# Optimization experiments

Hardware: AMD Instinct MI355X
Metric: run time of the kernel (lower is better)

## Reference

```python
import jax, jax.numpy as jnp
import numpy as np

B, T, N = 128, 20, 49
VOCAB, EMB, HDIM, VDIM, ATT = 10000, 512, 1024, 512, 512
LN_EPS = 1e-5


def _layer_norm(x, g, b):
    mu = x.mean(-1, keepdims=True)
    var = ((x - mu) ** 2).mean(-1, keepdims=True)
    return (x - mu) * jax.lax.rsqrt(var + LN_EPS) * g + b


def _lstm_cell(x, h, c, Wih, Whh, bih, bhh):
    gates = x @ Wih.T + h @ Whh.T + bih + bhh  # [B, 4H]
    i, f, g, o = jnp.split(gates, 4, axis=-1)  # torch LSTMCell gate order
    c_new = jax.nn.sigmoid(f) * c + jax.nn.sigmoid(i) * jnp.tanh(g)
    h_new = jax.nn.sigmoid(o) * jnp.tanh(c_new)
    return h_new, c_new


def setup_inputs() -> dict:
    key = jax.random.key(0)
    ks = jax.random.split(key, 16)
    w = lambda k, shape: (jax.random.normal(k, shape, jnp.float32) * 0.02)
    embed_W = w(ks[2], (VOCAB, EMB)).at[0].set(0.0)  # padding_idx=0 row is zeros
    return dict(
        V=jax.random.normal(ks[0], (B, N, VDIM), jnp.float32),
        y=jax.random.randint(ks[1], (B, T), 0, VOCAB),
        embed_W=embed_W,
        Vp_W=w(ks[3], (HDIM, VDIM)), Vp_b=jnp.zeros((HDIM,), jnp.float32),
        attW=w(ks[4], (ATT, HDIM)), attU=w(ks[5], (ATT, HDIM)), attv=w(ks[6], (1, ATT)),
        l1_Wih=w(ks[7], (4 * HDIM, EMB + HDIM)), l1_Whh=w(ks[8], (4 * HDIM, HDIM)),
        l1_bih=jnp.zeros((4 * HDIM,), jnp.float32), l1_bhh=jnp.zeros((4 * HDIM,), jnp.float32),
        l2_Wih=w(ks[9], (4 * HDIM, HDIM)), l2_Whh=w(ks[10], (4 * HDIM, HDIM)),
        l2_bih=jnp.zeros((4 * HDIM,), jnp.float32), l2_bhh=jnp.zeros((4 * HDIM,), jnp.float32),
        n1_g=jnp.ones((HDIM,), jnp.float32), n1_b=jnp.zeros((HDIM,), jnp.float32),
        n2_g=jnp.ones((HDIM,), jnp.float32), n2_b=jnp.zeros((HDIM,), jnp.float32),
        ih_W=w(ks[11], (HDIM, HDIM)), ih_b=jnp.zeros((HDIM,), jnp.float32),
        ic_W=w(ks[12], (HDIM, HDIM)), ic_b=jnp.zeros((HDIM,), jnp.float32),
        proj_W=w(ks[13], (EMB, HDIM)),
    )


def reference(V, y, embed_W, Vp_W, Vp_b, attW, attU, attv,
              l1_Wih, l1_Whh, l1_bih, l1_bhh,
              l2_Wih, l2_Whh, l2_bih, l2_bhh,
              n1_g, n1_b, n2_g, n2_b,
              ih_W, ih_b, ic_W, ic_b, proj_W):
    Vp = V @ Vp_W.T + Vp_b                      # [B, N, H]
    feat_mean = Vp.mean(1)                      # [B, H]
    h1 = jnp.tanh(feat_mean @ ih_W.T + ih_b)
    c1 = jnp.tanh(feat_mean @ ic_W.T + ic_b)
    h2 = jnp.zeros_like(h1)
    c2 = jnp.zeros_like(c1)

    Uv = Vp @ attU.T                            # [B, N, ATT] (hoisted out of loop)
    emb_y = embed_W[y]                          # [B, T, EMB]
    xs = jnp.swapaxes(emb_y[:, :-1], 0, 1)      # [T-1, B, EMB]

    def step(carry, x_t):
        h1, c1, h2, c2 = carry
        # additive attention (dropout is identity in eval)
        e = jnp.tanh((h2 @ attW.T)[:, None, :] + Uv) @ attv[0]   # [B, N]
        a = jax.nn.softmax(e, axis=1)
        ctx = jnp.einsum('bn,bnh->bh', a, Vp)
        h1n, c1n = _lstm_cell(jnp.concatenate([x_t, ctx], -1), h1, c1,
                              l1_Wih, l1_Whh, l1_bih, l1_bhh)
        h1n = _layer_norm(h1n, n1_g, n1_b)
        h2n, c2n = _lstm_cell(h1n, h2, c2, l2_Wih, l2_Whh, l2_bih, l2_bhh)
        h2n = _layer_norm(h2n, n2_g, n2_b)
        logit = (h2n @ proj_W.T) @ embed_W.T    # [B, VOCAB]
        return (h1n, c1n, h2n, c2n), logit

    _, logits = jax.lax.scan(step, (h1, c1, h2, c2), xs)
    return jnp.swapaxes(logits, 0, 1)           # [B, T-1, VOCAB]
```

## Files before the change

### kernel.cpp

```cpp
#include <hip/hip_runtime.h>
#include <hip/hip_bf16.h>

#define TSTEPS 19

typedef short bf16x8 __attribute__((ext_vector_type(8)));
typedef short bf16x4 __attribute__((ext_vector_type(4)));
typedef float f32x4 __attribute__((ext_vector_type(4)));

__device__ __forceinline__ f32x4 mfma_bf16(bf16x8 a, bf16x8 b, f32x4 c) {
    return __builtin_amdgcn_mfma_f32_16x16x32_bf16(a, b, c, 0, 0, 0);
}
__device__ __forceinline__ short f2b(float f) {
    union { float f; unsigned u; } v; v.f = f;
    unsigned r = v.u + 0x7fffu + ((v.u >> 16) & 1u);
    return (short)(r >> 16);
}
__device__ __forceinline__ float b2f(short s) {
    union { unsigned u; float f; } v; v.u = ((unsigned)(unsigned short)s) << 16;
    return v.f;
}
__device__ __forceinline__ float sigm(float x) { return 1.f / (1.f + __expf(-x)); }
__device__ __forceinline__ float tanhfast(float x) { return 1.f - 2.f / (__expf(2.f * x) + 1.f); }

__global__ __launch_bounds__(256) void k_convert(
    const float* __restrict__ l1_Wih, const float* __restrict__ l1_Whh,
    const float* __restrict__ l2_Wih, const float* __restrict__ l2_Whh,
    const float* __restrict__ embed_W, const float* __restrict__ proj_W,
    const float* __restrict__ attW, const float* __restrict__ ih_W,
    const float* __restrict__ ic_W, const float* __restrict__ Vp_W,
    const float* __restrict__ attU, const float* __restrict__ V,
    const int* __restrict__ y, const float* __restrict__ n1g,
    const float* __restrict__ n2g,
    short* __restrict__ l1h, short* __restrict__ l1l,
    short* __restrict__ l2h, short* __restrict__ l2l,
    short* __restrict__ embB, short* __restrict__ pa, short* __restrict__ ihic,
    short* __restrict__ VpWh, short* __restrict__ VpWl, short* __restrict__ attUb,
    short* __restrict__ Vbh, short* __restrict__ Vbl, short* __restrict__ xall) {
    const int N1 = 4096 * 2560, N2 = 4096 * 2048, N3 = 10000 * 512, N4 = 1024 * 1024,
              N5 = 2048 * 1024, N6 = 1024 * 512, N7 = 512 * 1024, N8 = 128 * 49 * 512,
              N9 = 19 * 128 * 512;
    const int total4 = (N1 + N2 + N3 + N4 + N5 + N6 + N7 + N8 + N9) >> 2;
    int stride = gridDim.x * blockDim.x;
    for (int g = blockIdx.x * blockDim.x + threadIdx.x; g < total4; g += stride) {
        int e = g << 2;
        if (e < N1) {
            int n = e / 2560, k = e - n * 2560;
            f32x4 v;
            if (k < 1536) {
                v = *(const f32x4*)(l1_Wih + (size_t)n * 1536 + k);
            } else {
                f32x4 w = *(const f32x4*)(l1_Whh + (size_t)n * 1024 + (k - 1536));
                f32x4 gg = *(const f32x4*)(n1g + (k - 1536));
#pragma unroll
                for (int j = 0; j < 4; j++) v[j] = gg[j] * w[j];
            }
            bf16x4 hi, lo;
#pragma unroll
            for (int j = 0; j < 4; j++) { hi[j] = f2b(v[j]); lo[j] = f2b(v[j] - b2f(hi[j])); }
            *(bf16x4*)(l1h + e) = hi; *(bf16x4*)(l1l + e) = lo; continue;
        }
        e -= N1;
        if (e < N2) {
            int n = e >> 11, k = e & 2047;
            f32x4 w, gg;
            if (k < 1024) {
                w = *(const f32x4*)(l2_Wih + (size_t)n * 1024 + k);
                gg = *(const f32x4*)(n1g + k);
            } else {
                w = *(const f32x4*)(l2_Whh + (size_t)n * 1024 + (k - 1024));
                gg = *(const f32x4*)(n2g + (k - 1024));
            }
            bf16x4 hi, lo;
#pragma unroll
            for (int j = 0; j < 4; j++) {
                float v = gg[j] * w[j];
                hi[j] = f2b(v); lo[j] = f2b(v - b2f(hi[j]));
            }
            *(bf16x4*)(l2h + e) = hi; *(bf16x4*)(l2l + e) = lo; continue;
        }
        e -= N2;
        if (e < N3) {
            f32x4 v = *(const f32x4*)(embed_W + e);
            bf16x4 o;
#pragma unroll
            for (int j = 0; j < 4; j++) o[j] = f2b(v[j]);
            *(bf16x4*)(embB + e) = o; continue;
        }
        e -= N3;
        if (e < N4) {
            int n = e >> 10, k = e & 1023;
            f32x4 w = (n < 512) ? *(const f32x4*)(proj_W + (size_t)n * 1024 + k)
                                : *(const f32x4*)(attW + (size_t)(n - 512) * 1024 + k);
            f32x4 gg = *(const f32x4*)(n2g + k);
            bf16x4 o;
#pragma unroll
            for (int j = 0; j < 4; j++) o[j] = f2b(gg[j] * w[j]);
            *(bf16x4*)(pa + e) = o; continue;
        }
        e -= N4;
        if (e < N5) {
            int n = e >> 10, k = e & 1023;
            f32x4 w = (n < 1024) ? *(const f32x4*)(ih_W + (size_t)n * 1024 + k)
                                 : *(const f32x4*)(ic_W + (size_t)(n - 1024) * 1024 + k);
            bf16x4 o;
#pragma unroll
            for (int j = 0; j < 4; j++) o[j] = f2b(w[j]);
            *(bf16x4*)(ihic + e) = o; continue;
        }
        e -= N5;
        if (e < N6) {
            f32x4 v = *(const f32x4*)(Vp_W + e);
            bf16x4 hi, lo;
#pragma unroll
            for (int j = 0; j < 4; j++) { hi[j] = f2b(v[j]); lo[j] = f2b(v[j] - b2f(hi[j])); }
            *(bf16x4*)(VpWh + e) = hi; *(bf16x4*)(VpWl + e) = lo; continue;
        }
        e -= N6;
        if (e < N7) {
            f32x4 v = *(const f32x4*)(attU + e);
            bf16x4 o;
#pragma unroll
            for (int j = 0; j < 4; j++) o[j] = f2b(v[j]);
            *(bf16x4*)(attUb + e) = o; continue;
        }
        e -= N7;
        if (e < N8) {
            f32x4 v = *(const f32x4*)(V + e);
            bf16x4 hi, lo;
#pragma unroll
            for (int j = 0; j < 4; j++) { hi[j] = f2b(v[j]); lo[j] = f2b(v[j] - b2f(hi[j])); }
            *(bf16x4*)(Vbh + e) = hi; *(bf16x4*)(Vbl + e) = lo; continue;
        }
        e -= N8;
        {
            int t = e >> 16; int r = e & 65535;
            int b = r >> 9, k = r & 511;
            int idx = y[b * 20 + t];
            f32x4 v = *(const f32x4*)(embed_W + (size_t)idx * 512 + k);
            bf16x4 o;
#pragma unroll
            for (int j = 0; j < 4; j++) o[j] = f2b(v[j]);
            *(bf16x4*)(xall + e) = o;
        }
    }
}

__global__ __launch_bounds__(256) void k_corr(
    const float* __restrict__ l1_Whh, const float* __restrict__ l2_Wih,
    const float* __restrict__ l2_Whh, const float* __restrict__ proj_W,
    const float* __restrict__ attW,
    const float* __restrict__ n1g, const float* __restrict__ n1b,
    const float* __restrict__ n2g, const float* __restrict__ n2b,
    float* __restrict__ wg1, float* __restrict__ wb1,
    float* __restrict__ wg2a, float* __restrict__ wb2a,
    float* __restrict__ wg2b, float* __restrict__ wb2b,
    float* __restrict__ wgp, float* __restrict__ wbp) {
    int w = (blockIdx.x * 256 + threadIdx.x) >> 6;
    int lane = threadIdx.x & 63;
    if (w >= 13312) return;
    const float* row; const float* g; const float* b; float* og; float* ob;
    if (w < 4096)       { row = l1_Whh + (size_t)w * 1024; g = n1g; b = n1b; og = wg1 + w; ob = wb1 + w; }
    else if (w < 8192)  { int j = w - 4096; row = l2_Wih + (size_t)j * 1024; g = n1g; b = n1b; og = wg2a + j; ob = wb2a + j; }
    else if (w < 12288) { int j = w - 8192; row = l2_Whh + (size_t)j * 1024; g = n2g; b = n2b; og = wg2b + j; ob = wb2b + j; }
    else                { int j = w - 12288;
                          row = (j < 512) ? proj_W + (size_t)j * 1024 : attW + (size_t)(j - 512) * 1024;
                          g = n2g; b = n2b; og = wgp + j; ob = wbp + j; }
    float sg = 0.f, sb = 0.f;
    for (int k = lane; k < 1024; k += 64) { float wv = row[k]; sg += g[k] * wv; sb += b[k] * wv; }
#pragma unroll
    for (int o = 1; o < 64; o <<= 1) { sg += __shfl_xor(sg, o); sb += __shfl_xor(sb, o); }
    if (lane == 0) { *og = sg; *ob = sb; }
}

__device__ __forceinline__ void gemm_core(const short* __restrict__ A, int lda,
                                          const short* __restrict__ Bm, int ldb,
                                          int mb, int n0, int K, int Nlim,
                                          f32x4 acc[2][4]) {
    int lane = threadIdx.x & 63, wave = threadIdx.x >> 6;
    int col = lane & 15, quad = lane >> 4;
    const short* a0p = A + (size_t)(mb + wave * 32 + col) * lda + quad * 8;
    const short* a1p = a0p + (size_t)16 * lda;
    const short* bp[4];
#pragma unroll
    for (int s = 0; s < 4; s++) {
        int n = n0 + s * 16 + col;
        if (n >= Nlim) n = 0;
        bp[s] = Bm + (size_t)n * ldb + quad * 8;
    }
    for (int kb = 0; kb < K; kb += 32) {
        bf16x8 a0 = *(const bf16x8*)(a0p + kb);
        bf16x8 a1 = *(const bf16x8*)(a1p + kb);
#pragma unroll
        for (int s = 0; s < 4; s++) {
            bf16x8 b = *(const bf16x8*)(bp[s] + kb);
            acc[0][s] = mfma_bf16(a0, b, acc[0][s]);
            acc[1][s] = mfma_bf16(a1, b, acc[1][s]);
        }
    }
}

__global__ __launch_bounds__(256) void k_gemm_vp(const short* __restrict__ Ah,
                                                 const short* __restrict__ Al,
                                                 const short* __restrict__ Bh,
                                                 const short* __restrict__ Bl,
                                                 const float* __restrict__ Vp_b,
                                                 short* __restrict__ Vph,
                                                 short* __restrict__ Vpl) {
    __shared__ alignas(16) short Bs[2 * 64 * 256];
    char* Bsb = (char*)Bs;
    int tid = threadIdx.x, lane = tid & 63, wave = tid >> 6, col = lane & 15, quad = lane >> 4;
    int mb = blockIdx.y * 128, n0 = blockIdx.x * 64;
    f32x4 acc[2][4] = {};
    const short* ah0 = Ah + (size_t)(mb + wave * 32 + col) * 512 + quad * 8;
    const short* al0 = Al + (size_t)(mb + wave * 32 + col) * 512 + quad * 8;
    const short* ah1 = ah0 + 16 * 512; const short* al1 = al0 + 16 * 512;
#pragma unroll
    for (int ph = 0; ph < 2; ph++) {
        int kbase = ph * 256;
        __syncthreads();
#pragma unroll
        for (int i = 0; i < 8; i++) {
            int r = i * 8 + wave * 2 + (lane >> 5);
            int n = n0 + r;
            int e = (lane & 31) * 8;
            bf16x8 vh = *(const bf16x8*)(Bh + (size_t)n * 512 + kbase + e);
            bf16x8 vl = *(const bf16x8*)(Bl + (size_t)n * 512 + kbase + e);
            int wo = r * 512 + ((e * 2) ^ ((r & 7) << 4));
            *(bf16x8*)(Bsb + wo) = vh;
            *(bf16x8*)(Bsb + 32768 + wo) = vl;
        }
        __syncthreads();
        for (int kb = 0; kb < 256; kb += 32) {
            bf16x8 h0 = *(const bf16x8*)(ah0 + kbase + kb), l0 = *(const bf16x8*)(al0 + kbase + kb);
            bf16x8 h1 = *(const bf16x8*)(ah1 + kbase + kb), l1 = *(const bf16x8*)(al1 + kbase + kb);
#pragma unroll
            for (int s = 0; s < 4; s++) {
                int r = s * 16 + col;
                int off = r * 512 + ((quad * 16 + kb * 2) ^ ((r & 7) << 4));
                bf16x8 wh = *(const bf16x8*)(Bsb + off);
                bf16x8 wl = *(const bf16x8*)(Bsb + 32768 + off);
                acc[0][s] = mfma_bf16(h0, wh, acc[0][s]);
                acc[0][s] = mfma_bf16(l0, wh, acc[0][s]);
                acc[0][s] = mfma_bf16(h0, wl, acc[0][s]);
                acc[1][s] = mfma_bf16(h1, wh, acc[1][s]);
                acc[1][s] = mfma_bf16(l1, wh, acc[1][s]);
                acc[1][s] = mfma_bf16(h1, wl, acc[1][s]);
            }
        }
    }
#pragma unroll
    for (int i = 0; i < 2; i++)
#pragma unroll
        for (int s = 0; s < 4; s++) {
            int n = n0 + s * 16 + col;
            float bias = Vp_b[n];
#pragma unroll
            for (int r = 0; r < 4; r++) {
                int m = mb + wave * 32 + i * 16 + quad * 4 + r;
                float v = acc[i][s][r] + bias;
                short hi = f2b(v);
                Vph[(size_t)m * 1024 + n] = hi;
                Vpl[(size_t)m * 1024 + n] = f2b(v - b2f(hi));
            }
        }
}

__global__ __launch_bounds__(256) void k_gemm_uv(const short* __restrict__ Vph,
                                                 const short* __restrict__ Vpl,
                                                 const short* __restrict__ attUb,
                                                 short* __restrict__ Uv) {
    __shared__ alignas(16) short Bs[64 * 512];
    char* Bsb = (char*)Bs;
    int tid = threadIdx.x, lane = tid & 63, wave = tid >> 6, col = lane & 15, quad = lane >> 4;
    int mb = blockIdx.y * 128, n0 = blockIdx.x * 64;
    f32x4 acc[2][4] = {};
    const short* ah0 = Vph + (size_t)(mb + wave * 32 + col) * 1024 + quad * 8;
    const short* al0 = Vpl + (size_t)(mb + wave * 32 + col) * 1024 + quad * 8;
    const short* ah1 = ah0 + 16 * 1024; const short* al1 = al0 + 16 * 1024;
#pragma unroll
    for (int ph = 0; ph < 2; ph++) {
        int kbase = ph * 512;
        __syncthreads();
#pragma unroll
        for (int i = 0; i < 16; i++) {
            int r = i * 4 + wave;
            int n = n0 + r;
            int e = lane * 8;
            bf16x8 v = *(const bf16x8*)(attUb + (size_t)n * 1024 + kbase + e);
            *(bf16x8*)(Bsb + r * 1024 + ((e * 2) ^ ((r & 7) << 4))) = v;
        }
        __syncthreads();
        for (int kb = 0; kb < 512; kb += 32) {
            bf16x8 h0 = *(const bf16x8*)(ah0 + kbase + kb), l0 = *(const bf16x8*)(al0 + kbase + kb);
            bf16x8 h1 = *(const bf16x8*)(ah1 + kbase + kb), l1 = *(const bf16x8*)(al1 + kbase + kb);
#pragma unroll
            for (int s = 0; s < 4; s++) {
                int r = s * 16 + col;
                bf16x8 b = *(const bf16x8*)(Bsb + r * 1024 + ((quad * 16 + kb * 2) ^ ((r & 7) << 4)));
                acc[0][s] = mfma_bf16(h0, b, acc[0][s]);
                acc[0][s] = mfma_bf16(l0, b, acc[0][s]);
                acc[1][s] = mfma_bf16(h1, b, acc[1][s]);
                acc[1][s] = mfma_bf16(l1, b, acc[1][s]);
            }
        }
    }
#pragma unroll
    for (int i = 0; i < 2; i++)
#pragma unroll
        for (int s = 0; s < 4; s++) {
            int n = n0 + s * 16 + col;
#pragma unroll
            for (int r = 0; r < 4; r++) {
                int m = mb + wave * 32 + i * 16 + quad * 4 + r;
                Uv[(size_t)m * 512 + n] = f2b(acc[i][s][r]);
            }
        }
}

__global__ __launch_bounds__(256) void k_gemm_xpart(const short* __restrict__ xall,
                                                    const short* __restrict__ l1h,
                                                    float* __restrict__ xpart) {
    f32x4 acc[2][4] = {};
    int mb = blockIdx.y * 128, n0 = blockIdx.x * 64;
    gemm_core(xall, 512, l1h, 2560, mb, n0, 512, 1 << 30, acc);
    int lane = threadIdx.x & 63, wave = threadIdx.x >> 6, col = lane & 15, quad = lane >> 4;
#pragma unroll
    for (int i = 0; i < 2; i++)
#pragma unroll
        for (int s = 0; s < 4; s++) {
            int n = n0 + s * 16 + col;
#pragma unroll
            for (int r = 0; r < 4; r++) {
                int m = mb + wave * 32 + i * 16 + quad * 4 + r;
                xpart[(size_t)m * 4096 + n] = acc[i][s][r];
            }
        }
}

__global__ __launch_bounds__(256) void k_feat(const short* __restrict__ Vph,
                                              const short* __restrict__ Vpl,
                                              short* __restrict__ feat,
                                              float* __restrict__ c2,
                                              short* __restrict__ h2h1,
                                              short* __restrict__ h2l1,
                                              float* __restrict__ st1,
                                              float* __restrict__ st2) {
    int b = blockIdx.x, tid = threadIdx.x;
    int h0 = tid * 4;
    float acc[4] = {0.f, 0.f, 0.f, 0.f};
    for (int n = 0; n < 49; n++) {
        bf16x4 vh = *(const bf16x4*)(Vph + ((size_t)b * 49 + n) * 1024 + h0);
        bf16x4 vl = *(const bf16x4*)(Vpl + ((size_t)b * 49 + n) * 1024 + h0);
#pragma unroll
        for (int j = 0; j < 4; j++) acc[j] += b2f(vh[j]) + b2f(vl[j]);
    }
    bf16x4 o;
#pragma unroll
    for (int j = 0; j < 4; j++) o[j] = f2b(acc[j] * (1.f / 49.f));
    *(bf16x4*)(feat + (size_t)b * 1024 + h0) = o;
#pragma unroll
    for (int j = 0; j < 4; j++) {
        c2[(size_t)b * 1024 + h0 + j] = 0.f;
        h2h1[(size_t)b * 1024 + h0 + j] = 0;
        h2l1[(size_t)b * 1024 + h0 + j] = 0;
    }
    if (tid == 0) {
        st1[(128 + b) * 2] = 0.f; st1[(128 + b) * 2 + 1] = 1.f;
        st2[(128 + b) * 2] = 0.f; st2[(128 + b) * 2 + 1] = 1.f;
    }
}

__global__ __launch_bounds__(256) void k_gemm_h1c1(const short* __restrict__ feat,
                                                   const short* __restrict__ ihic,
                                                   const float* __restrict__ ih_b,
                                                   const float* __restrict__ ic_b,
                                                   short* __restrict__ h1h1,
                                                   short* __restrict__ h1l1,
                                                   float* __restrict__ c1) {
    f32x4 acc[2][4] = {};
    int n0 = blockIdx.y * 64;
    gemm_core(feat, 1024, ihic, 1024, 0, n0, 1024, 1 << 30, acc);
    int lane = threadIdx.x & 63, wave = threadIdx.x >> 6, col = lane & 15, quad = lane >> 4;
#pragma unroll
    for (int i = 0; i < 2; i++)
#pragma unroll
        for (int s = 0; s < 4; s++) {
            int n = n0 + s * 16 + col;
#pragma unroll
            for (int r = 0; r < 4; r++) {
                int m = wave * 32 + i * 16 + quad * 4 + r;
                float v = acc[i][s][r];
                if (n < 1024) {
                    float t = tanhfast(v + ih_b[n]);
                    short hi = f2b(t);
                    h1h1[(size_t)m * 1024 + n] = hi;
                    h1l1[(size_t)m * 1024 + n] = f2b(t - b2f(hi));
                } else {
                    c1[(size_t)m * 1024 + (n - 1024)] = tanhfast(v + ic_b[n - 1024]);
                }
            }
        }
}

__global__ __launch_bounds__(256) void k_attn(
        int t,
        const float* __restrict__ pproj,
        const float* __restrict__ st2p,
        const float* __restrict__ wgp, const float* __restrict__ wbp,
        short* __restrict__ pbuf_prev,
        const short* __restrict__ Uv,
        const float* __restrict__ attv, const short* __restrict__ Vph,
        const short* __restrict__ Vpl,
        short* __restrict__ ctxh, short* __restrict__ ctxl) {
    int b = blockIdx.x, tid = threadIdx.x;
    int lane = tid & 63, wave = tid >> 6;
    __shared__ float shW[512];
    __shared__ float se[49], sa[49];
    if (t == 0) {
        shW[tid] = 0.f; shW[tid + 256] = 0.f;
    } else {
        float mu = st2p[b * 2], rs = st2p[b * 2 + 1];
        int n4 = tid * 4;
        f32x4 p0 = *(const f32x4*)(pproj + (size_t)b * 1024 + n4);
        f32x4 p1 = *(const f32x4*)(pproj + 131072 + (size_t)b * 1024 + n4);
        f32x4 wb = *(const f32x4*)(wbp + n4);
        f32x4 wg = *(const f32x4*)(wgp + n4);
        float v[4];
#pragma unroll
        for (int j = 0; j < 4; j++) v[j] = rs * (p0[j] + p1[j]) + wb[j] - rs * mu * wg[j];
        if (n4 < 512) {
            bf16x4 o;
#pragma unroll
            for (int j = 0; j < 4; j++) o[j] = f2b(v[j]);
            *(bf16x4*)(pbuf_prev + (size_t)b * 512 + n4) = o;
        } else {
#pragma unroll
            for (int j = 0; j < 4; j++) shW[n4 - 512 + j] = v[j];
        }
    }
    __syncthreads();
    for (int n = wave; n < 49; n += 4) {
        const float* hw = shW + lane * 8;
        const short* uv = Uv + ((size_t)b * 49 + n) * 512 + lane * 8;
        const float* av = attv + lane * 8;
        bf16x8 u8 = *(const bf16x8*)uv;
        float part = 0.f;
#pragma unroll
        for (int j = 0; j < 8; j++) part += tanhfast(hw[j] + b2f(u8[j])) * av[j];
#pragma unroll
        for (int o = 1; o < 64; o <<= 1) part += __shfl_xor(part, o);
        if (lane == 0) se[n] = part;
    }
    __syncthreads();
    if (wave == 0) {
        float v = (lane < 49) ? se[lane] : -1e30f;
        float mx = v;
#pragma unroll
        for (int o = 1; o < 64; o <<= 1) mx = fmaxf(mx, __shfl_xor(mx, o));
        float p = (lane < 49) ? __expf(v - mx) : 0.f;
        float s = p;
#pragma unroll
        for (int o = 1; o < 64; o <<= 1) s += __shfl_xor(s, o);
        if (lane < 49) sa[lane] = p / s;
    }
    __syncthreads();
    {
        int h0 = tid * 4;
        float acc[4] = {0.f, 0.f, 0.f, 0.f};
        for (int n = 0; n < 49; n++) {
            float wgt = sa[n];
            bf16x4 vh = *(const bf16x4*)(Vph + ((size_t)b * 49 + n) * 1024 + h0);
            bf16x4 vl = *(const bf16x4*)(Vpl + ((size_t)b * 49 + n) * 1024 + h0);
#pragma unroll
            for (int j = 0; j < 4; j++) acc[j] += wgt * (b2f(vh[j]) + b2f(vl[j]));
        }
        bf16x4 oh, ol;
#pragma unroll
        for (int j = 0; j < 4; j++) {
            short hi = f2b(acc[j]); oh[j] = hi; ol[j] = f2b(acc[j] - b2f(hi));
        }
        *(bf16x4*)(ctxh + (size_t)b * 1024 + h0) = oh;
        *(bf16x4*)(ctxl + (size_t)b * 1024 + h0) = ol;
    }
}

__global__ __launch_bounds__(256) void k_lstm1_mm(
        const short* __restrict__ ctxh, const short* __restrict__ ctxl,
        const short* __restrict__ h1hp, const short* __restrict__ h1lp,
        const short* __restrict__ l1h, const short* __restrict__ l1l,
        float* __restrict__ part) {
    __shared__ alignas(16) short Bs[2 * 64 * 256];
    char* Bsb = (char*)Bs;
    int bn = blockIdx.x, bk = blockIdx.y;
    int tid = threadIdx.x, lane = tid & 63, wave = tid >> 6, col = lane & 15, quad = lane >> 4;
    int n0 = bn * 64;
    int kw0 = 512 + bk * 256;
#pragma unroll
    for (int i = 0; i < 8; i++) {
        int r = i * 8 + wave * 2 + (lane >> 5);
        int e = (lane & 31) * 8;
        size_t src = (size_t)(n0 + r) * 2560 + kw0 + e;
        bf16x8 vh = *(const bf16x8*)(l1h + src);
        bf16x8 vl = *(const bf16x8*)(l1l + src);
        int wo = r * 512 + ((e * 2) ^ ((r & 7) << 4));
        *(bf16x8*)(Bsb + wo) = vh;
        *(bf16x8*)(Bsb + 32768 + wo) = vl;
    }
    __syncthreads();
    f32x4 acc[2][4] = {};
    int r0 = wave * 32 + col;
    const short* Ah = (bk < 4) ? ctxh : h1hp;
    const short* Al = (bk < 4) ? ctxl : h1lp;
    int ko = (bk & 3) * 256;
    const short* a0h = Ah + (size_t)r0 * 1024 + ko + quad * 8;
    const short* a0l = Al + (size_t)r0 * 1024 + ko + quad * 8;
    const short* a1h = a0h + 16 * 1024; const short* a1l = a0l + 16 * 1024;
    for (int kb = 0; kb < 256; kb += 32) {
        bf16x8 h0 = *(const bf16x8*)(a0h + kb), l0 = *(const bf16x8*)(a0l + kb);
        bf16x8 h1 = *(const bf16x8*)(a1h + kb), l1 = *(const bf16x8*)(a1l + kb);
#pragma unroll
        for (int s = 0; s < 4; s++) {
            int r = s * 16 + col;
            int off = r * 512 + ((quad * 16 + kb * 2) ^ ((r & 7) << 4));
            bf16x8 wh = *(const bf16x8*)(Bsb + off);
            bf16x8 wl = *(const bf16x8*)(Bsb + 32768 + off);
            acc[0][s] = mfma_bf16(h0, wh, acc[0][s]);
            acc[0][s] = mfma_bf16(l0, wh, acc[0][s]);
            acc[0][s] = mfma_bf16(h0, wl, acc[0][s]);
            acc[1][s] = mfma_bf16(h1, wh, acc[1][s]);
            acc[1][s] = mfma_bf16(l1, wh, acc[1][s]);
            acc[1][s] = mfma_bf16(h1, wl, acc[1][s]);
        }
    }
#pragma unroll
    for (int i = 0; i < 2; i++)
#pragma unroll
        for (int s = 0; s < 4; s++)
#pragma unroll
            for (int r = 0; r < 4; r++) {
                int m = wave * 32 + i * 16 + quad * 4 + r;
                part[((size_t)bk * 128 + m) * 4096 + n0 + s * 16 + col] = acc[i][s][r];
            }
}

__global__ __launch_bounds__(256) void k_red1(const float* __restrict__ part,
        const float* __restrict__ xpart_t,
        const float* __restrict__ st_prev,
        const float* __restrict__ wg1, const float* __restrict__ wb1,
        const float* __restrict__ bih, const float* __restrict__ bhh,
        float* __restrict__ c1, short* __restrict__ h1hc, short* __restrict__ h1lc,
        float* __restrict__ st_cur) {
    int m = blockIdx.x, tid = threadIdx.x;
    float mu_p = st_prev[m * 2], rs_p = st_prev[m * 2 + 1];
    const size_t SB = 128UL * 4096;
    int h = tid * 4;
    float pre[4][4];
#pragma unroll
    for (int g = 0; g < 4; g++) {
        int n = g * 1024 + h;
        size_t base = (size_t)m * 4096 + n;
        f32x4 pA = *(const f32x4*)(xpart_t + base);
        f32x4 pB = {};
#pragma unroll
        for (int q = 0; q < 4; q++) {
            f32x4 pa_ = *(const f32x4*)(part + q * SB + base);
            f32x4 pb_ = *(const f32x4*)(part + (q + 4) * SB + base);
#pragma unroll
            for (int j = 0; j < 4; j++) { pA[j] += pa_[j]; pB[j] += pb_[j]; }
        }
        f32x4 wb = *(const f32x4*)(wb1 + n);
        f32x4 wg = *(const f32x4*)(wg1 + n);
        f32x4 bi = *(const f32x4*)(bih + n);
        f32x4 bh = *(const f32x4*)(bhh + n);
#pragma unroll
        for (int j = 0; j < 4; j++)
            pre[g][j] = pA[j] + rs_p * pB[j] + wb[j] - rs_p * mu_p * wg[j] + bi[j] + bh[j];
    }
    size_t idx = (size_t)m * 1024 + h;
    f32x4 cv = *(const f32x4*)(c1 + idx);
    f32x4 cn_v; bf16x4 oh, ol;
    float s1 = 0.f, s2 = 0.f;
#pragma unroll
    for (int j = 0; j < 4; j++) {
        float cn = sigm(pre[1][j]) * cv[j] + sigm(pre[0][j]) * tanhfast(pre[2][j]);
        float hn = sigm(pre[3][j]) * tanhfast(cn);
        cn_v[j] = cn;
        short hi = f2b(hn); oh[j] = hi; ol[j] = f2b(hn - b2f(hi));
        s1 += hn; s2 += hn * hn;
    }
    *(f32x4*)(c1 + idx) = cn_v;
    *(bf16x4*)(h1hc + idx) = oh;
    *(bf16x4*)(h1lc + idx) = ol;
    __shared__ float red[8];
    int lane = tid & 63, wave = tid >> 6;
#pragma unroll
    for (int o = 1; o < 64; o <<= 1) { s1 += __shfl_xor(s1, o); s2 += __shfl_xor(s2, o); }
    if (lane == 0) { red[wave * 2] = s1; red[wave * 2 + 1] = s2; }
    __syncthreads();
    if (tid == 0) {
        float S1 = red[0] + red[2] + red[4] + red[6];
        float S2 = red[1] + red[3] + red[5] + red[7];
        float mu = S1 * (1.f / 1024.f);
        float var = S2 * (1.f / 1024.f) - mu * mu;
        st_cur[m * 2] = mu; st_cur[m * 2 + 1] = rsqrtf(var + 1e-5f);
    }
}

__global__ __launch_bounds__(256) void k_lstm2_mm(
        const short* __restrict__ h1hc, const short* __restrict__ h1lc,
        const short* __restrict__ h2hp, const short* __restrict__ h2lp,
        const short* __restrict__ l2h, const short* __restrict__ l2l,
        float* __restrict__ part) {
    __shared__ alignas(16) short Bs[2 * 64 * 256];
    char* Bsb = (char*)Bs;
    int bn = blockIdx.x, bk = blockIdx.y;
    int tid = threadIdx.x, lane = tid & 63, wave = tid >> 6, col = lane & 15, quad = lane >> 4;
    int n0 = bn * 64;
    int kw0 = bk * 256;
#pragma unroll
    for (int i = 0; i < 8; i++) {
        int r = i * 8 + wave * 2 + (lane >> 5);
        int e = (lane & 31) * 8;
        size_t src = (size_t)(n0 + r) * 2048 + kw0 + e;
        bf16x8 vh = *(const bf16x8*)(l2h + src);
        bf16x8 vl = *(const bf16x8*)(l2l + src);
        int wo = r * 512 + ((e * 2) ^ ((r & 7) << 4));
        *(bf16x8*)(Bsb + wo) = vh;
        *(bf16x8*)(Bsb + 32768 + wo) = vl;
    }
    __syncthreads();
    f32x4 acc[2][4] = {};
    int r0 = wave * 32 + col;
    const short* Ah = (bk < 4) ? h1hc : h2hp;
    const short* Al = (bk < 4) ? h1lc : h2lp;
    int ko = (bk & 3) * 256;
    const short* a0h = Ah + (size_t)r0 * 1024 + ko + quad * 8;
    const short* a0l = Al + (size_t)r0 * 1024 + ko + quad * 8;
    const short* a1h = a0h + 16 * 1024; const short* a1l = a0l + 16 * 1024;
    for (int kb = 0; kb < 256; kb += 32) {
        bf16x8 h0 = *(const bf16x8*)(a0h + kb), l0 = *(const bf16x8*)(a0l + kb);
        bf16x8 h1 = *(const bf16x8*)(a1h + kb), l1 = *(const bf16x8*)(a1l + kb);
#pragma unroll
        for (int s = 0; s < 4; s++) {
            int r = s * 16 + col;
            int off = r * 512 + ((quad * 16 + kb * 2) ^ ((r & 7) << 4));
            bf16x8 wh = *(const bf16x8*)(Bsb + off);
            bf16x8 wl = *(const bf16x8*)(Bsb + 32768 + off);
            acc[0][s] = mfma_bf16(h0, wh, acc[0][s]);
            acc[0][s] = mfma_bf16(l0, wh, acc[0][s]);
            acc[0][s] = mfma_bf16(h0, wl, acc[0][s]);
            acc[1][s] = mfma_bf16(h1, wh, acc[1][s]);
            acc[1][s] = mfma_bf16(l1, wh, acc[1][s]);
            acc[1][s] = mfma_bf16(h1, wl, acc[1][s]);
        }
    }
#pragma unroll
    for (int i = 0; i < 2; i++)
#pragma unroll
        for (int s = 0; s < 4; s++)
#pragma unroll
            for (int r = 0; r < 4; r++) {
                int m = wave * 32 + i * 16 + quad * 4 + r;
                part[((size_t)bk * 128 + m) * 4096 + n0 + s * 16 + col] = acc[i][s][r];
            }
}

__global__ __launch_bounds__(256) void k_red2(const float* __restrict__ part,
        const float* __restrict__ stA, const float* __restrict__ stB,
        const float* __restrict__ wg2a, const float* __restrict__ wb2a,
        const float* __restrict__ wg2b, const float* __restrict__ wb2b,
        const float* __restrict__ bih, const float* __restrict__ bhh,
        float* __restrict__ c2, short* __restrict__ h2hc, short* __restrict__ h2lc,
        float* __restrict__ st_cur) {
    int m = blockIdx.x, tid = threadIdx.x;
    float mu1 = stA[m * 2], rs1 = stA[m * 2 + 1];
    float mu2 = stB[m * 2], rs2 = stB[m * 2 + 1];
    const size_t SB = 128UL * 4096;
    int h = tid * 4;
    float pre[4][4];
#pragma unroll
    for (int g = 0; g < 4; g++) {
        int n = g * 1024 + h;
        size_t base = (size_t)m * 4096 + n;
        f32x4 pA = {}, pB = {};
#pragma unroll
        for (int q = 0; q < 4; q++) {
            f32x4 pa_ = *(const f32x4*)(part + q * SB + base);
            f32x4 pb_ = *(const f32x4*)(part + (q + 4) * SB + base);
#pragma unroll
            for (int j = 0; j < 4; j++) { pA[j] += pa_[j]; pB[j] += pb_[j]; }
        }
        f32x4 wba = *(const f32x4*)(wb2a + n);
        f32x4 wga = *(const f32x4*)(wg2a + n);
        f32x4 wbb = *(const f32x4*)(wb2b + n);
        f32x4 wgb = *(const f32x4*)(wg2b + n);
        f32x4 bi = *(const f32x4*)(bih + n);
        f32x4 bh = *(const f32x4*)(bhh + n);
#pragma unroll
        for (int j = 0; j < 4; j++)
            pre[g][j] = rs1 * pA[j] + rs2 * pB[j]
                        + wba[j] - rs1 * mu1 * wga[j]
                        + wbb[j] - rs2 * mu2 * wgb[j] + bi[j] + bh[j];
    }
    size_t idx = (size_t)m * 1024 + h;
    f32x4 cv = *(const f32x4*)(c2 + idx);
    f32x4 cn_v; bf16x4 oh, ol;
    float s1 = 0.f, s2 = 0.f;
#pragma unroll
    for (int j = 0; j < 4; j++) {
        float cn = sigm(pre[1][j]) * cv[j] + sigm(pre[0][j]) * tanhfast(pre[2][j]);
        float hn = sigm(pre[3][j]) * tanhfast(cn);
        cn_v[j] = cn;
        short hi = f2b(hn); oh[j] = hi; ol[j] = f2b(hn - b2f(hi));
        s1 += hn; s2 += hn * hn;
    }
    *(f32x4*)(c2 + idx) = cn_v;
    *(bf16x4*)(h2hc + idx) = oh;
    *(bf16x4*)(h2lc + idx) = ol;
    __shared__ float red[8];
    int lane = tid & 63, wave = tid >> 6;
#pragma unroll
    for (int o = 1; o < 64; o <<= 1) { s1 += __shfl_xor(s1, o); s2 += __shfl_xor(s2, o); }
    if (lane == 0) { red[wave * 2] = s1; red[wave * 2 + 1] = s2; }
    __syncthreads();
    if (tid == 0) {
        float S1 = red[0] + red[2] + red[4] + red[6];
        float S2 = red[1] + red[3] + red[5] + red[7];
        float mu = S1 * (1.f / 1024.f);
        float var = S2 * (1.f / 1024.f) - mu * mu;
        st_cur[m * 2] = mu; st_cur[m * 2 + 1] = rsqrtf(var + 1e-5f);
    }
}

__global__ __launch_bounds__(256) void k_projatt(
        const short* __restrict__ h2hc, const short* __restrict__ h2lc,
        const short* __restrict__ pa,
        float* __restrict__ pproj) {
    int nt = blockIdx.x, mh = blockIdx.y, kc = blockIdx.z;
    int tid = threadIdx.x, lane = tid & 63, wave = tid >> 6, col = lane & 15, quad = lane >> 4;
    int arow = mh * 64 + wave * 16 + col;
    int n = nt * 16 + col;
    int k0 = kc * 512;
    f32x4 acc = {};
    const short* bp = pa + (size_t)n * 1024 + k0 + quad * 8;
    const short* ah = h2hc + (size_t)arow * 1024 + k0 + quad * 8;
    const short* al = h2lc + (size_t)arow * 1024 + k0 + quad * 8;
    for (int kb = 0; kb < 512; kb += 32) {
        bf16x8 xh = *(const bf16x8*)(ah + kb);
        bf16x8 xl = *(const bf16x8*)(al + kb);
        bf16x8 b = *(const bf16x8*)(bp + kb);
        acc = mfma_bf16(xh, b, acc);
        acc = mfma_bf16(xl, b, acc);
    }
#pragma unroll
    for (int r = 0; r < 4; r++) {
        int m = mh * 64 + wave * 16 + quad * 4 + r;
        pproj[(size_t)kc * 131072 + (size_t)m * 1024 + nt * 16 + col] = acc[r];
    }
}

__global__ __launch_bounds__(256) void k_pbuf(const float* __restrict__ pproj,
        const float* __restrict__ st2c,
        const float* __restrict__ wgp, const float* __restrict__ wbp,
        short* __restrict__ pbuf) {
    int b = blockIdx.x, tid = threadIdx.x;
    float mu = st2c[b * 2], rs = st2c[b * 2 + 1];
#pragma unroll
    for (int j = 0; j < 2; j++) {
        int n = tid * 2 + j;
        float v = rs * (pproj[(size_t)b * 1024 + n] + pproj[131072 + (size_t)b * 1024 + n])
                  + wbp[n] - rs * mu * wgp[n];
        pbuf[(size_t)b * 512 + n] = f2b(v);
    }
}

__global__ __launch_bounds__(256) void k_logits_all(const short* __restrict__ pbuf_all,
                                                    const short* __restrict__ embB,
                                                    float* __restrict__ out) {
    int n0 = blockIdx.x * 64, t = blockIdx.y;
    __shared__ alignas(16) short Bs[64 * 512];
    char* Bsb = (char*)Bs;
    int tid = threadIdx.x, lane = tid & 63, wave = tid >> 6;
#pragma unroll
    for (int i = 0; i < 16; i++) {
        int r = i * 4 + wave;
        int n = n0 + r; if (n >= 10000) n = 0;
        bf16x8 v = *(const bf16x8*)(embB + (size_t)n * 512 + lane * 8);
        *(bf16x8*)(Bsb + r * 1024 + ((lane * 16) ^ ((r & 7) << 4))) = v;
    }
    __syncthreads();
    int col = lane & 15, quad = lane >> 4;
    f32x4 acc[2][4] = {};
    const short* A = pbuf_all + (size_t)t * 128 * 512;
    const short* a0p = A + (size_t)(wave * 32 + col) * 512 + quad * 8;
    const short* a1p = a0p + 16 * 512;
    int rbase[4], rkey[4];
#pragma unroll
    for (int s = 0; s < 4; s++) {
        int r = s * 16 + col;
        rbase[s] = r * 1024;
        rkey[s] = (r & 7) << 4;
    }
#pragma unroll 4
    for (int kb = 0; kb < 512; kb += 32) {
        bf16x8 a0 = *(const bf16x8*)(a0p + kb);
        bf16x8 a1 = *(const bf16x8*)(a1p + kb);
#pragma unroll
        for (int s = 0; s < 4; s++) {
            bf16x8 bfrag = *(const bf16x8*)(Bsb + rbase[s] + ((quad * 16 + kb * 2) ^ rkey[s]));
            acc[0][s] = mfma_bf16(a0, bfrag, acc[0][s]);
            acc[1][s] = mfma_bf16(a1, bfrag, acc[1][s]);
        }
    }
#pragma unroll
    for (int i = 0; i < 2; i++)
#pragma unroll
        for (int s = 0; s < 4; s++) {
            int n = n0 + s * 16 + col;
            if (n >= 10000) continue;
#pragma unroll
            for (int r = 0; r < 4; r++) {
                int m = wave * 32 + i * 16 + quad * 4 + r;
                out[((size_t)m * 19 + t) * 10000 + n] = acc[i][s][r];
            }
        }
}

extern "C" void kernel_launch(void* const* d_in, const int* in_sizes, int n_in,
                              void* d_out, int out_size, void* d_ws, size_t ws_size,
                              hipStream_t stream) {
    const float* V = (const float*)d_in[0];
    const int* y = (const int*)d_in[1];
    const float* embed_W = (const float*)d_in[2];
    const float* Vp_W = (const float*)d_in[3];
    const float* Vp_b = (const float*)d_in[4];
    const float* attW = (const float*)d_in[5];
    const float* attU = (const float*)d_in[6];
    const float* attv = (const float*)d_in[7];
    const float* l1_Wih = (const float*)d_in[8];
    const float* l1_Whh = (const float*)d_in[9];
    const float* l1_bih = (const float*)d_in[10];
    const float* l1_bhh = (const float*)d_in[11];
    const float* l2_Wih = (const float*)d_in[12];
    const float* l2_Whh = (const float*)d_in[13];
    const float* l2_bih = (const float*)d_in[14];
    const float* l2_bhh = (const float*)d_in[15];
    const float* n1g = (const float*)d_in[16];
    const float* n1b = (const float*)d_in[17];
    const float* n2g = (const float*)d_in[18];
    const float* n2b = (const float*)d_in[19];
    const float* ih_W = (const float*)d_in[20];
    const float* ih_b = (const float*)d_in[21];
    const float* ic_W = (const float*)d_in[22];
    const float* ic_b = (const float*)d_in[23];
    const float* proj_W = (const float*)d_in[24];
    float* out = (float*)d_out;
    (void)in_sizes; (void)n_in; (void)out_size;

    char* wsp = (char*)d_ws;
    size_t off = 0;
    auto alloc = [&](size_t bytes) -> void* {
        void* p = wsp + off;
        off += (bytes + 255) & ~(size_t)255;
        return p;
    };
    short* l1h  = (short*)alloc(4096UL * 2560 * 2);
    short* l1l  = (short*)alloc(4096UL * 2560 * 2);
    short* l2h  = (short*)alloc(4096UL * 2048 * 2);
    short* l2l  = (short*)alloc(4096UL * 2048 * 2);
    short* embB = (short*)alloc(10000UL * 512 * 2);
    short* pa   = (short*)alloc(1024UL * 1024 * 2);
    short* ihic = (short*)alloc(2048UL * 1024 * 2);
    short* VpWh = (short*)alloc(1024UL * 512 * 2);
    short* VpWl = (short*)alloc(1024UL * 512 * 2);
    short* attUb= (short*)alloc(512UL * 1024 * 2);
    short* Vbh  = (short*)alloc(128UL * 49 * 512 * 2);
    short* Vbl  = (short*)alloc(128UL * 49 * 512 * 2);
    short* xall = (short*)alloc(19UL * 128 * 512 * 2);
    short* Vph  = (short*)alloc(6272UL * 1024 * 2);
    short* Vpl  = (short*)alloc(6272UL * 1024 * 2);
    short* Uv   = (short*)alloc(6272UL * 512 * 2);
    short* feat = (short*)alloc(128UL * 1024 * 2);
    short* ctxh = (short*)alloc(128UL * 1024 * 2);
    short* ctxl = (short*)alloc(128UL * 1024 * 2);
    short* h1h  = (short*)alloc(2UL * 128 * 1024 * 2);
    short* h1l  = (short*)alloc(2UL * 128 * 1024 * 2);
    short* h2h  = (short*)alloc(2UL * 128 * 1024 * 2);
    short* h2l  = (short*)alloc(2UL * 128 * 1024 * 2);
    short* pbuf_all = (short*)alloc(19UL * 128 * 512 * 2);
    float* c1   = (float*)alloc(128UL * 1024 * 4);
    float* c2   = (float*)alloc(128UL * 1024 * 4);
    float* st1  = (float*)alloc(2UL * 128 * 2 * 4);
    float* st2  = (float*)alloc(2UL * 128 * 2 * 4);
    float* pmm  = (float*)alloc(8UL * 128 * 4096 * 4);
    float* pproj= (float*)alloc(2UL * 128 * 1024 * 4);
    float* xpart= (float*)alloc(2432UL * 4096 * 4);
    float* wg1  = (float*)alloc(4096UL * 4);
    float* wb1  = (float*)alloc(4096UL * 4);
    float* wg2a = (float*)alloc(4096UL * 4);
    float* wb2a = (float*)alloc(4096UL * 4);
    float* wg2b = (float*)alloc(4096UL * 4);
    float* wb2b = (float*)alloc(4096UL * 4);
    float* wgp  = (float*)alloc(1024UL * 4);
    float* wbp  = (float*)alloc(1024UL * 4);
    if (off > ws_size) return;

    const size_t HB = 128UL * 1024;
    const size_t SB2 = 128UL * 2;

    k_convert<<<2048, 256, 0, stream>>>(l1_Wih, l1_Whh, l2_Wih, l2_Whh, embed_W, proj_W,
                                        attW, ih_W, ic_W, Vp_W, attU, V, y, n1g, n2g,
                                        l1h, l1l, l2h, l2l, embB, pa, ihic,
                                        VpWh, VpWl, attUb, Vbh, Vbl, xall);
    k_corr<<<3328, 256, 0, stream>>>(l1_Whh, l2_Wih, l2_Whh, proj_W, attW,
                                     n1g, n1b, n2g, n2b,
                                     wg1, wb1, wg2a, wb2a, wg2b, wb2b, wgp, wbp);
    k_gemm_vp<<<dim3(16, 49), 256, 0, stream>>>(Vbh, Vbl, VpWh, VpWl, Vp_b, Vph, Vpl);
    k_gemm_xpart<<<dim3(64, 19), 256, 0, stream>>>(xall, l1h, xpart);
    k_feat<<<128, 256, 0, stream>>>(Vph, Vpl, feat, c2, h2h + HB, h2l + HB, st1, st2);
    k_gemm_h1c1<<<dim3(1, 32), 256, 0, stream>>>(feat, ihic, ih_b, ic_b,
                                                 h1h + HB, h1l + HB, c1);
    k_gemm_uv<<<dim3(8, 49), 256, 0, stream>>>(Vph, Vpl, attUb, Uv);

    for (int t = 0; t < TSTEPS; t++) {
        int cur = t & 1, prev = cur ^ 1;
        short* pbuf_prev = pbuf_all + (size_t)(t > 0 ? t - 1 : 0) * 128 * 512;
        k_attn<<<128, 256, 0, stream>>>(t, pproj, st2 + prev * SB2, wgp, wbp,
                                        pbuf_prev, Uv, attv, Vph, Vpl, ctxh, ctxl);
        k_lstm1_mm<<<dim3(64, 8), 256, 0, stream>>>(ctxh, ctxl,
                                                    h1h + prev * HB, h1l + prev * HB,
                                                    l1h, l1l, pmm);
        k_red1<<<128, 256, 0, stream>>>(pmm, xpart + (size_t)t * 128 * 4096,
                                        st1 + prev * SB2, wg1, wb1,
                                        l1_bih, l1_bhh, c1,
                                        h1h + cur * HB, h1l + cur * HB, st1 + cur * SB2);
        k_lstm2_mm<<<dim3(64, 8), 256, 0, stream>>>(h1h + cur * HB, h1l + cur * HB,
                                                    h2h + prev * HB, h2l + prev * HB,
                                                    l2h, l2l, pmm);
        k_red2<<<128, 256, 0, stream>>>(pmm, st1 + cur * SB2, st2 + prev * SB2,
                                        wg2a, wb2a, wg2b, wb2b, l2_bih, l2_bhh, c2,
                                        h2h + cur * HB, h2l + cur * HB, st2 + cur * SB2);
        k_projatt<<<dim3(64, 2, 2), 256, 0, stream>>>(h2h + cur * HB, h2l + cur * HB,
                                                      pa, pproj);
    }
    k_pbuf<<<128, 256, 0, stream>>>(pproj, st2, wgp, wbp,
                                    pbuf_all + 18UL * 128 * 512);
    k_logits_all<<<dim3(157, 19), 256, 0, stream>>>(pbuf_all, embB, out);
}
```

Baseline: 1.958 ms.

## Split LSTM weight staging into halves and remap logits blocks per XCD

In both LSTM matmul kernels, all global weight loads now go into registers up front, but only the first half of the tile is written to LDS before compute starts. The second half is stored after the first half's MFMAs finish, so global load latency overlaps with compute at the cost of an extra barrier and more register pressure. The logits kernel moves to a 1D grid and remaps block IDs so consecutive work items for the same embedding tile land on the same XCD, aiming for better L2 reuse of embedding rows across timesteps.

```diff
diff --git a/kernel.cpp b/kernel.cpp
--- a/kernel.cpp
+++ b/kernel.cpp
@@ -495,16 +495,28 @@
     int tid = threadIdx.x, lane = tid & 63, wave = tid >> 6, col = lane & 15, quad = lane >> 4;
     int n0 = bn * 64;
     int kw0 = 512 + bk * 256;
-#pragma unroll
-    for (int i = 0; i < 8; i++) {
+    bf16x8 hA[4], lA[4], hB[4], lB[4];
+#pragma unroll
+    for (int i = 0; i < 4; i++) {
+        int r = i * 8 + wave * 2 + (lane >> 5);
+        size_t src = (size_t)(n0 + r) * 2560 + kw0 + (lane & 31) * 8;
+        hA[i] = *(const bf16x8*)(l1h + src);
+        lA[i] = *(const bf16x8*)(l1l + src);
+    }
+#pragma unroll
+    for (int i = 0; i < 4; i++) {
+        int r = (i + 4) * 8 + wave * 2 + (lane >> 5);
+        size_t src = (size_t)(n0 + r) * 2560 + kw0 + (lane & 31) * 8;
+        hB[i] = *(const bf16x8*)(l1h + src);
+        lB[i] = *(const bf16x8*)(l1l + src);
+    }
+#pragma unroll
+    for (int i = 0; i < 4; i++) {
         int r = i * 8 + wave * 2 + (lane >> 5);
         int e = (lane & 31) * 8;
-        size_t src = (size_t)(n0 + r) * 2560 + kw0 + e;
-        bf16x8 vh = *(const bf16x8*)(l1h + src);
-        bf16x8 vl = *(const bf16x8*)(l1l + src);
         int wo = r * 512 + ((e * 2) ^ ((r & 7) << 4));
-        *(bf16x8*)(Bsb + wo) = vh;
-        *(bf16x8*)(Bsb + 32768 + wo) = vl;
+        *(bf16x8*)(Bsb + wo) = hA[i];
+        *(bf16x8*)(Bsb + 32768 + wo) = lA[i];
     }
     __syncthreads();
     f32x4 acc[2][4] = {};
@@ -519,7 +531,33 @@
         bf16x8 h0 = *(const bf16x8*)(a0h + kb), l0 = *(const bf16x8*)(a0l + kb);
         bf16x8 h1 = *(const bf16x8*)(a1h + kb), l1 = *(const bf16x8*)(a1l + kb);
 #pragma unroll
-        for (int s = 0; s < 4; s++) {
+        for (int s = 0; s < 2; s++) {
+            int r = s * 16 + col;
+            int off = r * 512 + ((quad * 16 + kb * 2) ^ ((r & 7) << 4));
+            bf16x8 wh = *(const bf16x8*)(Bsb + off);
+            bf16x8 wl = *(const bf16x8*)(Bsb + 32768 + off);
+            acc[0][s] = mfma_bf16(h0, wh, acc[0][s]);
+            acc[0][s] = mfma_bf16(l0, wh, acc[0][s]);
+            acc[0][s] = mfma_bf16(h0, wl, acc[0][s]);
+            acc[1][s] = mfma_bf16(h1, wh, acc[1][s]);
+            acc[1][s] = mfma_bf16(l1, wh, acc[1][s]);
+            acc[1][s] = mfma_bf16(h1, wl, acc[1][s]);
+        }
+    }
+#pragma unroll
+    for (int i = 0; i < 4; i++) {
+        int r = (i + 4) * 8 + wave * 2 + (lane >> 5);
+        int e = (lane & 31) * 8;
+        int wo = r * 512 + ((e * 2) ^ ((r & 7) << 4));
+        *(bf16x8*)(Bsb + wo) = hB[i];
+        *(bf16x8*)(Bsb + 32768 + wo) = lB[i];
+    }
+    __syncthreads();
+    for (int kb = 0; kb < 256; kb += 32) {
+        bf16x8 h0 = *(const bf16x8*)(a0h + kb), l0 = *(const bf16x8*)(a0l + kb);
+        bf16x8 h1 = *(const bf16x8*)(a1h + kb), l1 = *(const bf16x8*)(a1l + kb);
+#pragma unroll
+        for (int s = 2; s < 4; s++) {
             int r = s * 16 + col;
             int off = r * 512 + ((quad * 16 + kb * 2) ^ ((r & 7) << 4));
             bf16x8 wh = *(const bf16x8*)(Bsb + off);
@@ -617,16 +655,28 @@
     int tid = threadIdx.x, lane = tid & 63, wave = tid >> 6, col = lane & 15, quad = lane >> 4;
     int n0 = bn * 64;
     int kw0 = bk * 256;
-#pragma unroll
-    for (int i = 0; i < 8; i++) {
+    bf16x8 hA[4], lA[4], hB[4], lB[4];
+#pragma unroll
+    for (int i = 0; i < 4; i++) {
+        int r = i * 8 + wave * 2 + (lane >> 5);
+        size_t src = (size_t)(n0 + r) * 2048 + kw0 + (lane & 31) * 8;
+        hA[i] = *(const bf16x8*)(l2h + src);
+        lA[i] = *(const bf16x8*)(l2l + src);
+    }
+#pragma unroll
+    for (int i = 0; i < 4; i++) {
+        int r = (i + 4) * 8 + wave * 2 + (lane >> 5);
+        size_t src = (size_t)(n0 + r) * 2048 + kw0 + (lane & 31) * 8;
+        hB[i] = *(const bf16x8*)(l2h + src);
+        lB[i] = *(const bf16x8*)(l2l + src);
+    }
+#pragma unroll
+    for (int i = 0; i < 4; i++) {
         int r = i * 8 + wave * 2 + (lane >> 5);
         int e = (lane & 31) * 8;
-        size_t src = (size_t)(n0 + r) * 2048 + kw0 + e;
-        bf16x8 vh = *(const bf16x8*)(l2h + src);
-        bf16x8 vl = *(const bf16x8*)(l2l + src);
         int wo = r * 512 + ((e * 2) ^ ((r & 7) << 4));
-        *(bf16x8*)(Bsb + wo) = vh;
-        *(bf16x8*)(Bsb + 32768 + wo) = vl;
+        *(bf16x8*)(Bsb + wo) = hA[i];
+        *(bf16x8*)(Bsb + 32768 + wo) = lA[i];
     }
     __syncthreads();
     f32x4 acc[2][4] = {};
@@ -641,7 +691,33 @@
         bf16x8 h0 = *(const bf16x8*)(a0h + kb), l0 = *(const bf16x8*)(a0l + kb);
         bf16x8 h1 = *(const bf16x8*)(a1h + kb), l1 = *(const bf16x8*)(a1l + kb);
 #pragma unroll
-        for (int s = 0; s < 4; s++) {
+        for (int s = 0; s < 2; s++) {
+            int r = s * 16 + col;
+            int off = r * 512 + ((quad * 16 + kb * 2) ^ ((r & 7) << 4));
+            bf16x8 wh = *(const bf16x8*)(Bsb + off);
+            bf16x8 wl = *(const bf16x8*)(Bsb + 32768 + off);
+            acc[0][s] = mfma_bf16(h0, wh, acc[0][s]);
+            acc[0][s] = mfma_bf16(l0, wh, acc[0][s]);
+            acc[0][s] = mfma_bf16(h0, wl, acc[0][s]);
+            acc[1][s] = mfma_bf16(h1, wh, acc[1][s]);
+            acc[1][s] = mfma_bf16(l1, wh, acc[1][s]);
+            acc[1][s] = mfma_bf16(h1, wl, acc[1][s]);
+        }
+    }
+#pragma unroll
+    for (int i = 0; i < 4; i++) {
+        int r = (i + 4) * 8 + wave * 2 + (lane >> 5);
+        int e = (lane & 31) * 8;
+        int wo = r * 512 + ((e * 2) ^ ((r & 7) << 4));
+        *(bf16x8*)(Bsb + wo) = hB[i];
+        *(bf16x8*)(Bsb + 32768 + wo) = lB[i];
+    }
+    __syncthreads();
+    for (int kb = 0; kb < 256; kb += 32) {
+        bf16x8 h0 = *(const bf16x8*)(a0h + kb), l0 = *(const bf16x8*)(a0l + kb);
+        bf16x8 h1 = *(const bf16x8*)(a1h + kb), l1 = *(const bf16x8*)(a1l + kb);
+#pragma unroll
+        for (int s = 2; s < 4; s++) {
             int r = s * 16 + col;
             int off = r * 512 + ((quad * 16 + kb * 2) ^ ((r & 7) << 4));
             bf16x8 wh = *(const bf16x8*)(Bsb + off);
@@ -777,7 +853,12 @@
 __global__ __launch_bounds__(256) void k_logits_all(const short* __restrict__ pbuf_all,
                                                     const short* __restrict__ embB,
                                                     float* __restrict__ out) {
-    int n0 = blockIdx.x * 64, t = blockIdx.y;
+    const int NWG = 157 * 19, Q = NWG / 8, R8 = NWG % 8;
+    int orig = blockIdx.x;
+    int xcd = orig & 7, local = orig >> 3;
+    int wid = (xcd < R8 ? xcd * (Q + 1) : R8 * (Q + 1) + (xcd - R8) * Q) + local;
+    int nt = wid / 19, t = wid - nt * 19;
+    int n0 = nt * 64;
     __shared__ alignas(16) short Bs[64 * 512];
     char* Bsb = (char*)Bs;
     int tid = threadIdx.x, lane = tid & 63, wave = tid >> 6;
@@ -945,5 +1026,5 @@
     }
     k_pbuf<<<128, 256, 0, stream>>>(pproj, st2, wgp, wbp,
                                     pbuf_all + 18UL * 128 * 512);
-    k_logits_all<<<dim3(157, 19), 256, 0, stream>>>(pbuf_all, embB, out);
-}
+    k_logits_all<<<dim3(157 * 19), 256, 0, stream>>>(pbuf_all, embB, out);
+}
```

Measured after the change: 2.184 ms. +11.5%, slower.
